# Performance work log

Measured on AMD Instinct MI355X. Metric: run time of the kernel, lower is better.

The kernel has to match this reference:

```python
import jax, jax.numpy as jnp
import numpy as np

N = 30000      # nodes
E = 480000     # edges (avg degree 16)
IN = 128       # atom in_channels
ED = 16        # edge_dim
D = 128        # hidden_channels
OUT = 64       # out_channels
L = 4          # num_layers + 1 GCNEConv layers


def setup_inputs() -> dict:
    key = jax.random.key(0)
    ks = jax.random.split(key, 8)
    w = lambda k, sh: (jax.random.normal(k, sh, dtype=jnp.float32) * 0.05)
    return {
        "x": jax.random.normal(ks[0], (N, IN), dtype=jnp.float32),
        "edge_index": jax.random.randint(ks[1], (2, E), 0, N, dtype=jnp.int64),
        "edge_attr": jax.random.normal(ks[2], (E, ED), dtype=jnp.float32),
        "W_atom": w(ks[3], (IN, D)), "b_atom": jnp.zeros((D,), jnp.float32),
        "W_bond": w(ks[4], (ED, D)), "b_bond": jnp.zeros((D,), jnp.float32),
        "W_seq": w(ks[5], (L, D, D)), "b_seq": jnp.zeros((L, D), jnp.float32),
        "W_lin": w(ks[6], (2 * D, OUT)), "b_lin": jnp.zeros((OUT,), jnp.float32),
    }


def _aggregate(h_bond, idx_i, n):
    # CMPNN 'message_booster': elementwise sum_agg * max_agg over incoming edges
    sum_agg = jax.ops.segment_sum(h_bond, idx_i, num_segments=n)
    max_agg = jax.ops.segment_max(h_bond, idx_i, num_segments=n)
    max_agg = jnp.where(jnp.isfinite(max_agg), max_agg, 0.0)  # empty segments -> 0
    return sum_agg * max_agg


def reference(x, edge_index, edge_attr, W_atom, b_atom, W_bond, b_bond,
              W_seq, b_seq, W_lin, b_lin):
    n = x.shape[0]
    idx_i = edge_index[0]  # flow='target_to_source' -> i is edge_index[0]
    idx_j = edge_index[1]

    x_proj = jax.nn.relu(x @ W_atom + b_atom)          # [N, D]
    h_atom = x_proj
    h_bond = jax.nn.relu(edge_attr @ W_bond + b_bond)  # [E, D]

    # first L-1 convs: node update + edge update
    for l in range(L - 1):
        msg = _aggregate(h_bond, idx_i, n)             # [N, D]
        h_atom = h_atom * msg                          # inner_product communicator
        # edge_update: x[edge_index_i] - edge_attr[edge_index_j] (node-index gather
        # into edge tensor, faithful to the original code; valid since E > N)
        bond = h_atom[idx_i] - h_bond[idx_j]           # [E, D]
        h_bond = jax.nn.relu(bond @ W_seq[l] + b_seq[l])

    # last conv: only the node output is used downstream
    msg = _aggregate(h_bond, idx_i, n)
    aggr_atom_message = h_atom * msg

    # top-level communicator (inner_product): hidden_state * message
    h_atom = h_atom * aggr_atom_message
    out = jnp.concatenate([h_atom, x_proj], axis=1) @ W_lin + b_lin  # [N, OUT]
    return out
```

## Files before the change

### kernel.cpp

```cpp
#include <hip/hip_runtime.h>
#include <hip/hip_bf16.h>

#define DD 128
#define SCB 256
#define CE  512
#define CB  512

typedef __attribute__((ext_vector_type(8))) short bf16x8;
typedef __attribute__((ext_vector_type(4))) float f32x4;
typedef __attribute__((ext_vector_type(2))) _Float16 f16x2;
typedef __attribute__((ext_vector_type(8))) _Float16 f16x8;

__device__ __forceinline__ unsigned bf16_rne(float f) {
    unsigned u = __float_as_uint(f);
    return (u + 0x7fffu + ((u >> 16) & 1u)) >> 16;
}

__global__ __launch_bounds__(256)
void hist_kernel(const int* __restrict__ idx_i, int* __restrict__ cnt, int E)
{
    const int e = blockIdx.x * 256 + threadIdx.x;
    if (e < E) atomicAdd(&cnt[idx_i[e]], 1);
}

__global__ __launch_bounds__(SCB)
void scan1_kernel(const int* __restrict__ cnt, int* __restrict__ exc,
                  int* __restrict__ bsum, int n)
{
    __shared__ int s[SCB];
    const int i = blockIdx.x * SCB + (int)threadIdx.x;
    const int v = (i < n) ? cnt[i] : 0;
    s[threadIdx.x] = v;
    __syncthreads();
    #pragma unroll
    for (int off = 1; off < SCB; off <<= 1) {
        int t = (threadIdx.x >= off) ? s[threadIdx.x - off] : 0;
        __syncthreads();
        s[threadIdx.x] += t;
        __syncthreads();
    }
    if (i < n) exc[i] = s[threadIdx.x] - v;
    if (threadIdx.x == SCB - 1) bsum[blockIdx.x] = s[threadIdx.x];
}

__global__ __launch_bounds__(SCB)
void scan2_kernel(int* __restrict__ bsum, int nb)
{
    __shared__ int s[SCB];
    const int v = (threadIdx.x < nb) ? bsum[threadIdx.x] : 0;
    s[threadIdx.x] = v;
    __syncthreads();
    #pragma unroll
    for (int off = 1; off < SCB; off <<= 1) {
        int t = (threadIdx.x >= off) ? s[threadIdx.x - off] : 0;
        __syncthreads();
        s[threadIdx.x] += t;
        __syncthreads();
    }
    if (threadIdx.x < nb) bsum[threadIdx.x] = s[threadIdx.x] - v;
}

__global__ __launch_bounds__(SCB)
void scan3_kernel(int* __restrict__ exc, const int* __restrict__ bsum, int n)
{
    const int i = blockIdx.x * SCB + (int)threadIdx.x;
    if (i < n) exc[i] += bsum[i >> 8];
}

__global__ __launch_bounds__(256)
void scatter_kernel(const int* __restrict__ idx_i, const int* __restrict__ idx_j,
                    int* __restrict__ cursor, int* __restrict__ perm,
                    int* __restrict__ si, int* __restrict__ sj, int E)
{
    const int e = blockIdx.x * 256 + threadIdx.x;
    if (e < E) {
        const int n = idx_i[e];
        const int p = atomicAdd(&cursor[n], 1);
        perm[p] = e;
        si[p] = n;
        sj[p] = idx_j[e];
    }
}

__global__ __launch_bounds__(512, 4)
void gemm128_mfma_kernel(float* __restrict__ A0, const float* __restrict__ A1,
                         int nA, int nTotal,
                         const float* __restrict__ W, const float* __restrict__ bias,
                         int bias_limit, int do_relu, int update,
                         float* __restrict__ sum_agg, int* __restrict__ max_agg,
                         float* __restrict__ out0, float* __restrict__ out1,
                         int ntiles)
{
    __shared__ __align__(16) unsigned char SM[65536];
    char* const Ahi = (char*)SM;
    char* const Alo = (char*)SM + 32768;

    const int t = (int)threadIdx.x;
    const int w = t >> 6;
    const int l = t & 63;
    const int g = l >> 4;
    const int q = l & 15;
    const int colv = w * 16 + q;

    bf16x8 wh[4], wl[4];
    #pragma unroll
    for (int ks = 0; ks < 4; ++ks) {
        unsigned h8[8], l8[8];
        #pragma unroll
        for (int j = 0; j < 8; ++j) {
            const float w0 = W[(size_t)(ks * 32 + g * 8 + j) * DD + colv];
            const unsigned hb = bf16_rne(w0);
            h8[j] = hb;
            l8[j] = bf16_rne(w0 - __uint_as_float(hb << 16));
        }
        uint4 ph, pl;
        ph.x = h8[0] | (h8[1] << 16); ph.y = h8[2] | (h8[3] << 16);
        ph.z = h8[4] | (h8[5] << 16); ph.w = h8[6] | (h8[7] << 16);
        pl.x = l8[0] | (l8[1] << 16); pl.y = l8[2] | (l8[3] << 16);
        pl.z = l8[4] | (l8[5] << 16); pl.w = l8[6] | (l8[7] << 16);
        wh[ks] = *(bf16x8*)&ph;
        wl[ks] = *(bf16x8*)&pl;
    }
    const float bv = bias ? bias[colv] : 0.f;

    for (int tile = blockIdx.x; tile < ntiles; tile += gridDim.x) {
        const int e0 = tile * 128;
        __syncthreads();

        #pragma unroll
        for (int i = 0; i < 4; ++i) {
            const int task = t + i * 512;
            const int row  = task >> 4;
            const int c    = task & 15;
            const int rr = min(e0 + row, nTotal - 1);
            float d[8];
            if (rr < nA) {
                float* ph0 = A0 + (size_t)rr * DD + c * 8;
                const float4 a0 = *(const float4*)ph0;
                const float4 a1 = *(const float4*)(ph0 + 4);
                if (update) {
                    float* sp = sum_agg + (size_t)rr * DD + c * 8;
                    int*   mp = max_agg + (size_t)rr * DD + c * 8;
                    const float4 s0 = *(const float4*)sp;
                    const float4 s1 = *(const float4*)(sp + 4);
                    const int4   m0 = *(const int4*)mp;
                    const int4   m1 = *(const int4*)(mp + 4);
                    d[0] = a0.x * s0.x * __int_as_float(m0.x);
                    d[1] = a0.y * s0.y * __int_as_float(m0.y);
                    d[2] = a0.z * s0.z * __int_as_float(m0.z);
                    d[3] = a0.w * s0.w * __int_as_float(m0.w);
                    d[4] = a1.x * s1.x * __int_as_float(m1.x);
                    d[5] = a1.y * s1.y * __int_as_float(m1.y);
                    d[6] = a1.z * s1.z * __int_as_float(m1.z);
                    d[7] = a1.w * s1.w * __int_as_float(m1.w);
                    *(float4*)ph0       = make_float4(d[0], d[1], d[2], d[3]);
                    *(float4*)(ph0 + 4) = make_float4(d[4], d[5], d[6], d[7]);
                    *(float4*)sp       = make_float4(0.f, 0.f, 0.f, 0.f);
                    *(float4*)(sp + 4) = make_float4(0.f, 0.f, 0.f, 0.f);
                    *(int4*)mp       = make_int4(0, 0, 0, 0);
                    *(int4*)(mp + 4) = make_int4(0, 0, 0, 0);
                } else {
                    d[0] = a0.x; d[1] = a0.y; d[2] = a0.z; d[3] = a0.w;
                    d[4] = a1.x; d[5] = a1.y; d[6] = a1.z; d[7] = a1.w;
                }
            } else {
                const float* pa = A1 + (size_t)(rr - nA) * DD + c * 8;
                const float4 a0 = *(const float4*)pa;
                const float4 a1 = *(const float4*)(pa + 4);
                d[0] = a0.x; d[1] = a0.y; d[2] = a0.z; d[3] = a0.w;
                d[4] = a1.x; d[5] = a1.y; d[6] = a1.z; d[7] = a1.w;
            }
            unsigned h8[8], l8[8];
            #pragma unroll
            for (int j = 0; j < 8; ++j) {
                const unsigned hb = bf16_rne(d[j]);
                h8[j] = hb;
                l8[j] = bf16_rne(d[j] - __uint_as_float(hb << 16));
            }
            uint4 ph, pl;
            ph.x = h8[0] | (h8[1] << 16); ph.y = h8[2] | (h8[3] << 16);
            ph.z = h8[4] | (h8[5] << 16); ph.w = h8[6] | (h8[7] << 16);
            pl.x = l8[0] | (l8[1] << 16); pl.y = l8[2] | (l8[3] << 16);
            pl.z = l8[4] | (l8[5] << 16); pl.w = l8[6] | (l8[7] << 16);
            const int off = ((row * 256 + c * 16)) ^ ((row & 7) << 4);
            *(uint4*)(Ahi + off) = ph;
            *(uint4*)(Alo + off) = pl;
        }
        __syncthreads();

        f32x4 acc[8];
        const f32x4 zero = {0.f, 0.f, 0.f, 0.f};
        #pragma unroll
        for (int m = 0; m < 8; ++m) acc[m] = zero;

        #pragma unroll
        for (int ks = 0; ks < 4; ++ks) {
            const int kbyte = ks * 64 + g * 16;
            #pragma unroll
            for (int m = 0; m < 8; ++m) {
                const int row = m * 16 + q;
                const int off = (row * 256 + kbyte) ^ ((row & 7) << 4);
                const bf16x8 ah = *(const bf16x8*)(Ahi + off);
                const bf16x8 al = *(const bf16x8*)(Alo + off);
                acc[m] = __builtin_amdgcn_mfma_f32_16x16x32_bf16(ah, wh[ks], acc[m], 0, 0, 0);
                acc[m] = __builtin_amdgcn_mfma_f32_16x16x32_bf16(ah, wl[ks], acc[m], 0, 0, 0);
                acc[m] = __builtin_amdgcn_mfma_f32_16x16x32_bf16(al, wh[ks], acc[m], 0, 0, 0);
            }
        }

        #pragma unroll
        for (int m = 0; m < 8; ++m) {
            #pragma unroll
            for (int r = 0; r < 4; ++r) {
                const int row = e0 + m * 16 + g * 4 + r;
                if (row < nTotal) {
                    float v = acc[m][r] + ((row < bias_limit) ? bv : 0.f);
                    if (do_relu) v = fmaxf(v, 0.f);
                    out0[(size_t)row * DD + colv] = v;
                    if (out1) out1[(size_t)row * DD + colv] = v;
                }
            }
        }
    }
}

__global__ __launch_bounds__(512)
void bond_pass_kernel(const float* __restrict__ edge_attr,
                      const float* __restrict__ Wb, const float* __restrict__ bb,
                      const int* __restrict__ si, const int* __restrict__ perm,
                      float* __restrict__ h_head0,
                      float* __restrict__ sum_agg, int* __restrict__ max_agg,
                      int E, int N)
{
    __shared__ __align__(16) _Float16 ea_s[CB][16];
    __shared__ int si_s[CB], pm_s[CB];

    const int p0b = blockIdx.x * CB;
    if (p0b >= E) return;
    const int t = (int)threadIdx.x;

    for (int i = t; i < CB; i += 512) {
        const int p = min(p0b + i, E - 1);
        si_s[i] = si[p];
        pm_s[i] = perm[p];
    }
    for (int task = t; task < CB * 2; task += 512) {
        const int row = task >> 1;
        const int h8i = task & 1;
        const int p = min(p0b + row, E - 1);
        const int orig = perm[p];
        const float4 a0 = *(const float4*)(edge_attr + (size_t)orig * 16 + h8i * 8);
        const float4 a1 = *(const float4*)(edge_attr + (size_t)orig * 16 + h8i * 8 + 4);
        f16x8 hv;
        hv[0] = (_Float16)a0.x; hv[1] = (_Float16)a0.y;
        hv[2] = (_Float16)a0.z; hv[3] = (_Float16)a0.w;
        hv[4] = (_Float16)a1.x; hv[5] = (_Float16)a1.y;
        hv[6] = (_Float16)a1.z; hv[7] = (_Float16)a1.w;
        *(f16x8*)(&ea_s[row][h8i * 8]) = hv;
    }
    __syncthreads();

    const int w    = t >> 6;
    const int lane = t & 63;
    const int c    = lane * 2;
    const int q0   = w * 64;
    const int pg0  = p0b + q0;
    if (pg0 >= E) return;

    f16x2 w0h[8], w1h[8];
    #pragma unroll
    for (int k = 0; k < 8; ++k) {
        const float2 wa = *(const float2*)(Wb + (2 * k)     * DD + c);
        const float2 wb2 = *(const float2*)(Wb + (2 * k + 1) * DD + c);
        w0h[k][0] = (_Float16)wa.x; w0h[k][1] = (_Float16)wb2.x;
        w1h[k][0] = (_Float16)wa.y; w1h[k][1] = (_Float16)wb2.y;
    }
    const float2 bc = *(const float2*)(bb + c);

    const int firstNode = si_s[q0];
    const int lastNode  = si_s[q0 + 63];

    int curNode = firstNode;
    float2 rs = make_float2(0.f, 0.f), rm = make_float2(0.f, 0.f);

    #define BP_FLUSH()                                                           \
    {                                                                            \
        if (curNode == firstNode || curNode == lastNode) {                       \
            atomicAdd(&sum_agg[(size_t)curNode * DD + c],     rs.x);             \
            atomicAdd(&sum_agg[(size_t)curNode * DD + c + 1], rs.y);             \
            atomicMax(&max_agg[(size_t)curNode * DD + c],     __float_as_int(rm.x)); \
            atomicMax(&max_agg[(size_t)curNode * DD + c + 1], __float_as_int(rm.y)); \
        } else {                                                                 \
            *(float2*)(sum_agg + (size_t)curNode * DD + c) = rs;                 \
            *(int2*)(max_agg + (size_t)curNode * DD + c) =                       \
                make_int2(__float_as_int(rm.x), __float_as_int(rm.y));           \
        }                                                                        \
    }

    #pragma unroll 4
    for (int kk = 0; kk < 64; ++kk) {
        const int i = si_s[q0 + kk];
        if (i != curNode) {
            BP_FLUSH();
            curNode = i;
            rs = make_float2(0.f, 0.f);
            rm = make_float2(0.f, 0.f);
        }
        const f16x8 e0 = *(const f16x8*)(&ea_s[q0 + kk][0]);
        const f16x8 e1 = *(const f16x8*)(&ea_s[q0 + kk][8]);
        float ax = bc.x, ay = bc.y;
        f16x2 p2;
        p2[0] = e0[0]; p2[1] = e0[1];
        ax = __builtin_amdgcn_fdot2(p2, w0h[0], ax, false);
        ay = __builtin_amdgcn_fdot2(p2, w1h[0], ay, false);
        p2[0] = e0[2]; p2[1] = e0[3];
        ax = __builtin_amdgcn_fdot2(p2, w0h[1], ax, false);
        ay = __builtin_amdgcn_fdot2(p2, w1h[1], ay, false);
        p2[0] = e0[4]; p2[1] = e0[5];
        ax = __builtin_amdgcn_fdot2(p2, w0h[2], ax, false);
        ay = __builtin_amdgcn_fdot2(p2, w1h[2], ay, false);
        p2[0] = e0[6]; p2[1] = e0[7];
        ax = __builtin_amdgcn_fdot2(p2, w0h[3], ax, false);
        ay = __builtin_amdgcn_fdot2(p2, w1h[3], ay, false);
        p2[0] = e1[0]; p2[1] = e1[1];
        ax = __builtin_amdgcn_fdot2(p2, w0h[4], ax, false);
        ay = __builtin_amdgcn_fdot2(p2, w1h[4], ay, false);
        p2[0] = e1[2]; p2[1] = e1[3];
        ax = __builtin_amdgcn_fdot2(p2, w0h[5], ax, false);
        ay = __builtin_amdgcn_fdot2(p2, w1h[5], ay, false);
        p2[0] = e1[4]; p2[1] = e1[5];
        ax = __builtin_amdgcn_fdot2(p2, w0h[6], ax, false);
        ay = __builtin_amdgcn_fdot2(p2, w1h[6], ay, false);
        p2[0] = e1[6]; p2[1] = e1[7];
        ax = __builtin_amdgcn_fdot2(p2, w0h[7], ax, false);
        ay = __builtin_amdgcn_fdot2(p2, w1h[7], ay, false);
        float2 v;
        v.x = fmaxf(ax, 0.f);
        v.y = fmaxf(ay, 0.f);
        if (pg0 + kk >= E) { v.x = 0.f; v.y = 0.f; }
        rs.x += v.x; rs.y += v.y;
        rm.x = fmaxf(rm.x, v.x); rm.y = fmaxf(rm.y, v.y);
        if (pg0 + kk < E) {
            const int orig = pm_s[q0 + kk];
            if (orig < N) *(float2*)(h_head0 + (size_t)orig * DD + c) = v;
        }
    }
    BP_FLUSH();
    #undef BP_FLUSH
}

__global__ __launch_bounds__(512)
void edge_pass_kernel(const float* __restrict__ PQ,
                      const int* __restrict__ si, const int* __restrict__ sj,
                      const int* __restrict__ perm,
                      float* __restrict__ head_next, int store_head,
                      float* __restrict__ sum_agg, int* __restrict__ max_agg,
                      int E, int N)
{
    __shared__ int si_s[CE], sj_s[CE], pm_s[CE];
    const int p0b = blockIdx.x * CE;
    if (p0b >= E) return;
    const int t = (int)threadIdx.x;
    for (int i = t; i < CE; i += 512) {
        const int p = min(p0b + i, E - 1);
        si_s[i] = si[p];
        sj_s[i] = sj[p];
        pm_s[i] = perm[p];
    }
    __syncthreads();

    const int w    = t >> 6;
    const int lane = t & 63;
    const int c    = lane * 2;
    const int q0   = w * 64;
    const int pg0  = p0b + q0;
    if (pg0 >= E) return;

    const int firstNode = si_s[q0];
    const int lastNode  = si_s[q0 + 63];

    const float* __restrict__ Qbase = PQ + (size_t)N * DD + c;

    float2 qa = *(const float2*)(Qbase + (size_t)sj_s[q0 + 0] * DD);
    float2 qb = *(const float2*)(Qbase + (size_t)sj_s[q0 + 1] * DD);
    float2 qc = *(const float2*)(Qbase + (size_t)sj_s[q0 + 2] * DD);
    float2 qd = *(const float2*)(Qbase + (size_t)sj_s[q0 + 3] * DD);
    float2 qe = *(const float2*)(Qbase + (size_t)sj_s[q0 + 4] * DD);
    float2 qf = *(const float2*)(Qbase + (size_t)sj_s[q0 + 5] * DD);
    float2 qg = *(const float2*)(Qbase + (size_t)sj_s[q0 + 6] * DD);
    float2 qh = *(const float2*)(Qbase + (size_t)sj_s[q0 + 7] * DD);

    int curNode = firstNode;
    float2 Pi = *(const float2*)(PQ + (size_t)curNode * DD + c);
    float2 rs = make_float2(0.f, 0.f), rm = make_float2(0.f, 0.f);

    #define EP_FLUSH()                                                           \
    {                                                                            \
        if (curNode == firstNode || curNode == lastNode) {                       \
            atomicAdd(&sum_agg[(size_t)curNode * DD + c],     rs.x);             \
            atomicAdd(&sum_agg[(size_t)curNode * DD + c + 1], rs.y);             \
            atomicMax(&max_agg[(size_t)curNode * DD + c],     __float_as_int(rm.x)); \
            atomicMax(&max_agg[(size_t)curNode * DD + c + 1], __float_as_int(rm.y)); \
        } else {                                                                 \
            *(float2*)(sum_agg + (size_t)curNode * DD + c) = rs;                 \
            *(int2*)(max_agg + (size_t)curNode * DD + c) =                       \
                make_int2(__float_as_int(rm.x), __float_as_int(rm.y));           \
        }                                                                        \
    }

    #define EP_STEP(K, QREG)                                                     \
    {                                                                            \
        const int kk = (K);                                                      \
        const int i = si_s[q0 + kk];                                             \
        if (i != curNode) {                                                      \
            EP_FLUSH();                                                          \
            curNode = i;                                                         \
            Pi = *(const float2*)(PQ + (size_t)i * DD + c);                      \
            rs = make_float2(0.f, 0.f);                                          \
            rm = make_float2(0.f, 0.f);                                          \
        }                                                                        \
        float2 v;                                                                \
        v.x = fmaxf(Pi.x - QREG.x, 0.f);                                         \
        v.y = fmaxf(Pi.y - QREG.y, 0.f);                                         \
        if (pg0 + kk >= E) { v.x = 0.f; v.y = 0.f; }                             \
        rs.x += v.x; rs.y += v.y;                                                \
        rm.x = fmaxf(rm.x, v.x); rm.y = fmaxf(rm.y, v.y);                        \
        if (store_head && (pg0 + kk) < E) {                                      \
            const int orig = pm_s[q0 + kk];                                      \
            if (orig < N) *(float2*)(head_next + (size_t)orig * DD + c) = v;     \
        }                                                                        \
        if (kk + 8 < 64)                                                         \
            QREG = *(const float2*)(Qbase + (size_t)sj_s[q0 + kk + 8] * DD);     \
    }

    #pragma unroll
    for (int k = 0; k < 64; k += 8) {
        EP_STEP(k + 0, qa);
        EP_STEP(k + 1, qb);
        EP_STEP(k + 2, qc);
        EP_STEP(k + 3, qd);
        EP_STEP(k + 4, qe);
        EP_STEP(k + 5, qf);
        EP_STEP(k + 6, qg);
        EP_STEP(k + 7, qh);
    }
    EP_FLUSH();
    #undef EP_STEP
    #undef EP_FLUSH
}

__global__ __launch_bounds__(512, 2)
void final_mfma_kernel(const float* __restrict__ h, const float* __restrict__ sum_agg,
                       const int* __restrict__ max_agg, const float* __restrict__ xp,
                       const float* __restrict__ Wl, const float* __restrict__ bl,
                       float* __restrict__ out, int N)
{
    __shared__ __align__(16) unsigned char SM[65808];
    char*  const Whi = (char*)SM;
    char*  const Wlo = (char*)SM + 32768;
    float* const Wf  = (float*)SM;
    float* const bs  = (float*)(SM + 65536);

    const int t = (int)threadIdx.x;
    {
        const float4* Wg = (const float4*)Wl;
        float4* Wd = (float4*)Wf;
        #pragma unroll
        for (int i = 0; i < 8; ++i) Wd[t + i * 512] = Wg[t + i * 512];
        if (t < 64) bs[t] = bl[t];
    }
    __syncthreads();
    {
        const int col = t & 63;
        const int kb  = (t >> 6) * 32;
        float v[32];
        #pragma unroll
        for (int j = 0; j < 32; ++j) v[j] = Wf[(size_t)(kb + j) * 64 + col];
        __syncthreads();
        #pragma unroll
        for (int c = 0; c < 4; ++c) {
            unsigned h8[8], l8[8];
            #pragma unroll
            for (int j = 0; j < 8; ++j) {
                const float w0 = v[c * 8 + j];
                const unsigned hb = bf16_rne(w0);
                h8[j] = hb;
                l8[j] = bf16_rne(w0 - __uint_as_float(hb << 16));
            }
            uint4 ph, pl;
            ph.x = h8[0] | (h8[1] << 16); ph.y = h8[2] | (h8[3] << 16);
            ph.z = h8[4] | (h8[5] << 16); ph.w = h8[6] | (h8[7] << 16);
            pl.x = l8[0] | (l8[1] << 16); pl.y = l8[2] | (l8[3] << 16);
            pl.z = l8[4] | (l8[5] << 16); pl.w = l8[6] | (l8[7] << 16);
            const int off = (col * 512 + (kb + c * 8) * 2) ^ ((col & 7) << 4);
            *(uint4*)(Whi + off) = ph;
            *(uint4*)(Wlo + off) = pl;
        }
    }
    __syncthreads();

    const int w  = t >> 6;
    const int l  = t & 63;
    const int wm = w >> 1;
    const int wn = w & 1;
    const int g  = l >> 4;
    const int q  = l & 15;
    const int r0 = (int)blockIdx.x * 128;

    f32x4 acc[2][2];
    const f32x4 zero = {0.f, 0.f, 0.f, 0.f};
    acc[0][0] = zero; acc[0][1] = zero; acc[1][0] = zero; acc[1][1] = zero;

    #pragma unroll
    for (int ks = 0; ks < 8; ++ks) {
        const int kf = (ks & 3) * 32 + g * 8;
        bf16x8 ah[2], al[2];
        #pragma unroll
        for (int m = 0; m < 2; ++m) {
            const int rr = min(r0 + wm * 32 + m * 16 + q, N - 1);
            float d[8];
            if (ks < 4) {
                const float* ph = h       + (size_t)rr * DD + kf;
                const float* ps = sum_agg + (size_t)rr * DD + kf;
                const int*   pm = max_agg + (size_t)rr * DD + kf;
                const float4 a0 = *(const float4*)ph;
                const float4 a1 = *(const float4*)(ph + 4);
                const float4 s0 = *(const float4*)ps;
                const float4 s1 = *(const float4*)(ps + 4);
                const int4   i0 = *(const int4*)pm;
                const int4   i1 = *(const int4*)(pm + 4);
                d[0] = a0.x * a0.x * s0.x * __int_as_float(i0.x);
                d[1] = a0.y * a0.y * s0.y * __int_as_float(i0.y);
                d[2] = a0.z * a0.z * s0.z * __int_as_float(i0.z);
                d[3] = a0.w * a0.w * s0.w * __int_as_float(i0.w);
                d[4] = a1.x * a1.x * s1.x * __int_as_float(i1.x);
                d[5] = a1.y * a1.y * s1.y * __int_as_float(i1.y);
                d[6] = a1.z * a1.z * s1.z * __int_as_float(i1.z);
                d[7] = a1.w * a1.w * s1.w * __int_as_float(i1.w);
            } else {
                const float* pa = xp + (size_t)rr * DD + kf;
                const float4 a0 = *(const float4*)pa;
                const float4 a1 = *(const float4*)(pa + 4);
                d[0] = a0.x; d[1] = a0.y; d[2] = a0.z; d[3] = a0.w;
                d[4] = a1.x; d[5] = a1.y; d[6] = a1.z; d[7] = a1.w;
            }
            unsigned h8[8], l8[8];
            #pragma unroll
            for (int j = 0; j < 8; ++j) {
                const unsigned hb = bf16_rne(d[j]);
                h8[j] = hb;
                l8[j] = bf16_rne(d[j] - __uint_as_float(hb << 16));
            }
            uint4 ph2, pl2;
            ph2.x = h8[0] | (h8[1] << 16); ph2.y = h8[2] | (h8[3] << 16);
            ph2.z = h8[4] | (h8[5] << 16); ph2.w = h8[6] | (h8[7] << 16);
            pl2.x = l8[0] | (l8[1] << 16); pl2.y = l8[2] | (l8[3] << 16);
            pl2.z = l8[4] | (l8[5] << 16); pl2.w = l8[6] | (l8[7] << 16);
            ah[m] = *(bf16x8*)&ph2;
            al[m] = *(bf16x8*)&pl2;
        }
        bf16x8 bh[2], blo[2];
        #pragma unroll
        for (int n = 0; n < 2; ++n) {
            const int colv = wn * 32 + n * 16 + q;
            const int off = (colv * 512 + ks * 64 + g * 16) ^ ((colv & 7) << 4);
            bh[n]  = *(const bf16x8*)(Whi + off);
            blo[n] = *(const bf16x8*)(Wlo + off);
        }
        #pragma unroll
        for (int m = 0; m < 2; ++m)
            #pragma unroll
            for (int n = 0; n < 2; ++n) {
                acc[m][n] = __builtin_amdgcn_mfma_f32_16x16x32_bf16(ah[m], bh[n],  acc[m][n], 0, 0, 0);
                acc[m][n] = __builtin_amdgcn_mfma_f32_16x16x32_bf16(ah[m], blo[n], acc[m][n], 0, 0, 0);
                acc[m][n] = __builtin_amdgcn_mfma_f32_16x16x32_bf16(al[m], bh[n],  acc[m][n], 0, 0, 0);
            }
    }

    #pragma unroll
    for (int n = 0; n < 2; ++n) {
        const int colv = wn * 32 + n * 16 + q;
        const float bv = bs[colv];
        #pragma unroll
        for (int m = 0; m < 2; ++m) {
            #pragma unroll
            for (int r = 0; r < 4; ++r) {
                const int row = r0 + wm * 32 + m * 16 + g * 4 + r;
                if (row < N) out[(size_t)row * 64 + colv] = acc[m][n][r] + bv;
            }
        }
    }
}

extern "C" void kernel_launch(void* const* d_in, const int* in_sizes, int n_in,
                              void* d_out, int out_size, void* d_ws, size_t ws_size,
                              hipStream_t stream)
{
    const float* x         = (const float*)d_in[0];
    const int*   edge_idx  = (const int*)d_in[1];
    const float* edge_attr = (const float*)d_in[2];
    const float* W_atom    = (const float*)d_in[3];
    const float* b_atom    = (const float*)d_in[4];
    const float* W_bond    = (const float*)d_in[5];
    const float* b_bond    = (const float*)d_in[6];
    const float* W_seq     = (const float*)d_in[7];
    const float* b_seq     = (const float*)d_in[8];
    const float* W_lin     = (const float*)d_in[9];
    const float* b_lin     = (const float*)d_in[10];
    float* out = (float*)d_out;

    const int N = in_sizes[0] / DD;
    const int E = in_sizes[1] / 2;
    const int* idx_i = edge_idx;
    const int* idx_j = edge_idx + E;

    const size_t nd = (size_t)N * DD;
    float* ws      = (float*)d_ws;
    float* x_proj  = ws;
    float* h_atom  = x_proj + nd;
    float* head    = h_atom + nd;
    float* sum_agg = head + nd;
    int*   max_agg = (int*)(sum_agg + nd);
    float* PQ      = (float*)(max_agg + nd);
    int*   cnt     = (int*)(PQ + 2 * nd);
    int*   cursor  = cnt + N;
    int*   bsum    = cursor + N;
    int*   perm    = bsum + 256;
    int*   si      = perm + E;
    int*   sj      = si + E;

    hipMemsetAsync(cnt, 0, (size_t)N * 4, stream);
    hist_kernel<<<(E + 255) / 256, 256, 0, stream>>>(idx_i, cnt, E);
    const int nb_scan = (N + SCB - 1) / SCB;
    scan1_kernel<<<nb_scan, SCB, 0, stream>>>(cnt, cursor, bsum, N);
    scan2_kernel<<<1, SCB, 0, stream>>>(bsum, nb_scan);
    scan3_kernel<<<nb_scan, SCB, 0, stream>>>(cursor, bsum, N);
    scatter_kernel<<<(E + 255) / 256, 256, 0, stream>>>(idx_i, idx_j, cursor, perm, si, sj, E);

    hipMemsetAsync(sum_agg, 0, nd * 4, stream);
    hipMemsetAsync(max_agg, 0, nd * 4, stream);

    const int ntiles_n = (N + 127) / 128;
    gemm128_mfma_kernel<<<ntiles_n, 512, 0, stream>>>(
        (float*)x, x, N, N, W_atom, b_atom, N, 1, 0, nullptr, nullptr,
        x_proj, h_atom, ntiles_n);

    bond_pass_kernel<<<(E + CB - 1) / CB, 512, 0, stream>>>(
        edge_attr, W_bond, b_bond, si, perm, head, sum_agg, max_agg, E, N);

    const int ntiles_pq = (2 * N + 127) / 128;
    const int ep_blocks = (E + CE - 1) / CE;
    for (int l = 0; l < 3; ++l) {
        gemm128_mfma_kernel<<<ntiles_pq, 512, 0, stream>>>(
            h_atom, head, N, 2 * N, W_seq + (size_t)l * DD * DD,
            b_seq + (size_t)l * DD, N, 0, 1, sum_agg, max_agg,
            PQ, nullptr, ntiles_pq);
        edge_pass_kernel<<<ep_blocks, 512, 0, stream>>>(
            PQ, si, sj, perm, head, (l < 2) ? 1 : 0, sum_agg, max_agg, E, N);
    }

    final_mfma_kernel<<<(N + 127) / 128, 512, 0, stream>>>(
        h_atom, sum_agg, (const int*)max_agg, x_proj, W_lin, b_lin, out, N);
}
```

Measured before the change: 387.4 us.

## Fuse atom projection GEMM and bond pass into one launch

Merges the atom-projection GEMM and the bond-pass kernel into a single launch, assigning the first block range to GEMM tiles and the remainder to bond-pass tiles. The two stages are independent, so they can now run concurrently and one kernel launch and its tail drain are removed. The cost is a shared 64KB LDS allocation for every block and a launch bound of 4 blocks per CU, which may reduce occupancy for the bond-pass blocks that need far less LDS.

New measurement: 384.3 us. Within noise of the previous version (-0.8%).

```diff
diff --git a/kernel.cpp b/kernel.cpp
--- a/kernel.cpp
+++ b/kernel.cpp
@@ -224,129 +224,231 @@
     }
 }
 
-__global__ __launch_bounds__(512)
-void bond_pass_kernel(const float* __restrict__ edge_attr,
+__global__ __launch_bounds__(512, 4)
+void proj_bond_kernel(const float* __restrict__ x,
+                      const float* __restrict__ W, const float* __restrict__ bias,
+                      float* __restrict__ x_proj, float* __restrict__ h_atom,
+                      int Nn, int nTilesProj,
+                      const float* __restrict__ edge_attr,
                       const float* __restrict__ Wb, const float* __restrict__ bb,
                       const int* __restrict__ si, const int* __restrict__ perm,
                       float* __restrict__ h_head0,
                       float* __restrict__ sum_agg, int* __restrict__ max_agg,
-                      int E, int N)
-{
-    __shared__ __align__(16) _Float16 ea_s[CB][16];
-    __shared__ int si_s[CB], pm_s[CB];
-
-    const int p0b = blockIdx.x * CB;
-    if (p0b >= E) return;
+                      int E)
+{
+    __shared__ __align__(16) unsigned char SM[65536];
     const int t = (int)threadIdx.x;
 
-    for (int i = t; i < CB; i += 512) {
-        const int p = min(p0b + i, E - 1);
-        si_s[i] = si[p];
-        pm_s[i] = perm[p];
-    }
-    for (int task = t; task < CB * 2; task += 512) {
-        const int row = task >> 1;
-        const int h8i = task & 1;
-        const int p = min(p0b + row, E - 1);
-        const int orig = perm[p];
-        const float4 a0 = *(const float4*)(edge_attr + (size_t)orig * 16 + h8i * 8);
-        const float4 a1 = *(const float4*)(edge_attr + (size_t)orig * 16 + h8i * 8 + 4);
-        f16x8 hv;
-        hv[0] = (_Float16)a0.x; hv[1] = (_Float16)a0.y;
-        hv[2] = (_Float16)a0.z; hv[3] = (_Float16)a0.w;
-        hv[4] = (_Float16)a1.x; hv[5] = (_Float16)a1.y;
-        hv[6] = (_Float16)a1.z; hv[7] = (_Float16)a1.w;
-        *(f16x8*)(&ea_s[row][h8i * 8]) = hv;
-    }
-    __syncthreads();
-
-    const int w    = t >> 6;
-    const int lane = t & 63;
-    const int c    = lane * 2;
-    const int q0   = w * 64;
-    const int pg0  = p0b + q0;
-    if (pg0 >= E) return;
-
-    f16x2 w0h[8], w1h[8];
-    #pragma unroll
-    for (int k = 0; k < 8; ++k) {
-        const float2 wa = *(const float2*)(Wb + (2 * k)     * DD + c);
-        const float2 wb2 = *(const float2*)(Wb + (2 * k + 1) * DD + c);
-        w0h[k][0] = (_Float16)wa.x; w0h[k][1] = (_Float16)wb2.x;
-        w1h[k][0] = (_Float16)wa.y; w1h[k][1] = (_Float16)wb2.y;
-    }
-    const float2 bc = *(const float2*)(bb + c);
-
-    const int firstNode = si_s[q0];
-    const int lastNode  = si_s[q0 + 63];
-
-    int curNode = firstNode;
-    float2 rs = make_float2(0.f, 0.f), rm = make_float2(0.f, 0.f);
-
-    #define BP_FLUSH()                                                           \
-    {                                                                            \
-        if (curNode == firstNode || curNode == lastNode) {                       \
-            atomicAdd(&sum_agg[(size_t)curNode * DD + c],     rs.x);             \
-            atomicAdd(&sum_agg[(size_t)curNode * DD + c + 1], rs.y);             \
-            atomicMax(&max_agg[(size_t)curNode * DD + c],     __float_as_int(rm.x)); \
-            atomicMax(&max_agg[(size_t)curNode * DD + c + 1], __float_as_int(rm.y)); \
-        } else {                                                                 \
-            *(float2*)(sum_agg + (size_t)curNode * DD + c) = rs;                 \
-            *(int2*)(max_agg + (size_t)curNode * DD + c) =                       \
-                make_int2(__float_as_int(rm.x), __float_as_int(rm.y));           \
-        }                                                                        \
-    }
-
-    #pragma unroll 4
-    for (int kk = 0; kk < 64; ++kk) {
-        const int i = si_s[q0 + kk];
-        if (i != curNode) {
-            BP_FLUSH();
-            curNode = i;
-            rs = make_float2(0.f, 0.f);
-            rm = make_float2(0.f, 0.f);
-        }
-        const f16x8 e0 = *(const f16x8*)(&ea_s[q0 + kk][0]);
-        const f16x8 e1 = *(const f16x8*)(&ea_s[q0 + kk][8]);
-        float ax = bc.x, ay = bc.y;
-        f16x2 p2;
-        p2[0] = e0[0]; p2[1] = e0[1];
-        ax = __builtin_amdgcn_fdot2(p2, w0h[0], ax, false);
-        ay = __builtin_amdgcn_fdot2(p2, w1h[0], ay, false);
-        p2[0] = e0[2]; p2[1] = e0[3];
-        ax = __builtin_amdgcn_fdot2(p2, w0h[1], ax, false);
-        ay = __builtin_amdgcn_fdot2(p2, w1h[1], ay, false);
-        p2[0] = e0[4]; p2[1] = e0[5];
-        ax = __builtin_amdgcn_fdot2(p2, w0h[2], ax, false);
-        ay = __builtin_amdgcn_fdot2(p2, w1h[2], ay, false);
-        p2[0] = e0[6]; p2[1] = e0[7];
-        ax = __builtin_amdgcn_fdot2(p2, w0h[3], ax, false);
-        ay = __builtin_amdgcn_fdot2(p2, w1h[3], ay, false);
-        p2[0] = e1[0]; p2[1] = e1[1];
-        ax = __builtin_amdgcn_fdot2(p2, w0h[4], ax, false);
-        ay = __builtin_amdgcn_fdot2(p2, w1h[4], ay, false);
-        p2[0] = e1[2]; p2[1] = e1[3];
-        ax = __builtin_amdgcn_fdot2(p2, w0h[5], ax, false);
-        ay = __builtin_amdgcn_fdot2(p2, w1h[5], ay, false);
-        p2[0] = e1[4]; p2[1] = e1[5];
-        ax = __builtin_amdgcn_fdot2(p2, w0h[6], ax, false);
-        ay = __builtin_amdgcn_fdot2(p2, w1h[6], ay, false);
-        p2[0] = e1[6]; p2[1] = e1[7];
-        ax = __builtin_amdgcn_fdot2(p2, w0h[7], ax, false);
-        ay = __builtin_amdgcn_fdot2(p2, w1h[7], ay, false);
-        float2 v;
-        v.x = fmaxf(ax, 0.f);
-        v.y = fmaxf(ay, 0.f);
-        if (pg0 + kk >= E) { v.x = 0.f; v.y = 0.f; }
-        rs.x += v.x; rs.y += v.y;
-        rm.x = fmaxf(rm.x, v.x); rm.y = fmaxf(rm.y, v.y);
-        if (pg0 + kk < E) {
-            const int orig = pm_s[q0 + kk];
-            if (orig < N) *(float2*)(h_head0 + (size_t)orig * DD + c) = v;
-        }
-    }
-    BP_FLUSH();
-    #undef BP_FLUSH
+    if ((int)blockIdx.x < nTilesProj) {
+        char* const Ahi = (char*)SM;
+        char* const Alo = (char*)SM + 32768;
+        const int w = t >> 6;
+        const int l = t & 63;
+        const int g = l >> 4;
+        const int q = l & 15;
+        const int colv = w * 16 + q;
+
+        bf16x8 wh[4], wl[4];
+        #pragma unroll
+        for (int ks = 0; ks < 4; ++ks) {
+            unsigned h8[8], l8[8];
+            #pragma unroll
+            for (int j = 0; j < 8; ++j) {
+                const float w0 = W[(size_t)(ks * 32 + g * 8 + j) * DD + colv];
+                const unsigned hb = bf16_rne(w0);
+                h8[j] = hb;
+                l8[j] = bf16_rne(w0 - __uint_as_float(hb << 16));
+            }
+            uint4 ph, pl;
+            ph.x = h8[0] | (h8[1] << 16); ph.y = h8[2] | (h8[3] << 16);
+            ph.z = h8[4] | (h8[5] << 16); ph.w = h8[6] | (h8[7] << 16);
+            pl.x = l8[0] | (l8[1] << 16); pl.y = l8[2] | (l8[3] << 16);
+            pl.z = l8[4] | (l8[5] << 16); pl.w = l8[6] | (l8[7] << 16);
+            wh[ks] = *(bf16x8*)&ph;
+            wl[ks] = *(bf16x8*)&pl;
+        }
+        const float bv = bias[colv];
+
+        const int e0 = (int)blockIdx.x * 128;
+
+        #pragma unroll
+        for (int i = 0; i < 4; ++i) {
+            const int task = t + i * 512;
+            const int row  = task >> 4;
+            const int c    = task & 15;
+            const int rr = min(e0 + row, Nn - 1);
+            const float* pa = x + (size_t)rr * DD + c * 8;
+            const float4 a0 = *(const float4*)pa;
+            const float4 a1 = *(const float4*)(pa + 4);
+            float d[8] = {a0.x, a0.y, a0.z, a0.w, a1.x, a1.y, a1.z, a1.w};
+            unsigned h8[8], l8[8];
+            #pragma unroll
+            for (int j = 0; j < 8; ++j) {
+                const unsigned hb = bf16_rne(d[j]);
+                h8[j] = hb;
+                l8[j] = bf16_rne(d[j] - __uint_as_float(hb << 16));
+            }
+            uint4 ph, pl;
+            ph.x = h8[0] | (h8[1] << 16); ph.y = h8[2] | (h8[3] << 16);
+            ph.z = h8[4] | (h8[5] << 16); ph.w = h8[6] | (h8[7] << 16);
+            pl.x = l8[0] | (l8[1] << 16); pl.y = l8[2] | (l8[3] << 16);
+            pl.z = l8[4] | (l8[5] << 16); pl.w = l8[6] | (l8[7] << 16);
+            const int off = ((row * 256 + c * 16)) ^ ((row & 7) << 4);
+            *(uint4*)(Ahi + off) = ph;
+            *(uint4*)(Alo + off) = pl;
+        }
+        __syncthreads();
+
+        f32x4 acc[8];
+        const f32x4 zero = {0.f, 0.f, 0.f, 0.f};
+        #pragma unroll
+        for (int m = 0; m < 8; ++m) acc[m] = zero;
+
+        #pragma unroll
+        for (int ks = 0; ks < 4; ++ks) {
+            const int kbyte = ks * 64 + g * 16;
+            #pragma unroll
+            for (int m = 0; m < 8; ++m) {
+                const int row = m * 16 + q;
+                const int off = (row * 256 + kbyte) ^ ((row & 7) << 4);
+                const bf16x8 ah = *(const bf16x8*)(Ahi + off);
+                const bf16x8 al = *(const bf16x8*)(Alo + off);
+                acc[m] = __builtin_amdgcn_mfma_f32_16x16x32_bf16(ah, wh[ks], acc[m], 0, 0, 0);
+                acc[m] = __builtin_amdgcn_mfma_f32_16x16x32_bf16(ah, wl[ks], acc[m], 0, 0, 0);
+                acc[m] = __builtin_amdgcn_mfma_f32_16x16x32_bf16(al, wh[ks], acc[m], 0, 0, 0);
+            }
+        }
+
+        #pragma unroll
+        for (int m = 0; m < 8; ++m) {
+            #pragma unroll
+            for (int r = 0; r < 4; ++r) {
+                const int row = e0 + m * 16 + g * 4 + r;
+                if (row < Nn) {
+                    const float v = fmaxf(acc[m][r] + bv, 0.f);
+                    x_proj[(size_t)row * DD + colv] = v;
+                    h_atom[(size_t)row * DD + colv] = v;
+                }
+            }
+        }
+    } else {
+        _Float16* const ea_s = (_Float16*)SM;
+        int* const si_s = (int*)(SM + 16384);
+        int* const pm_s = (int*)(SM + 18432);
+
+        const int bid = (int)blockIdx.x - nTilesProj;
+        const int p0b = bid * CB;
+        if (p0b >= E) return;
+
+        for (int i = t; i < CB; i += 512) {
+            const int p = min(p0b + i, E - 1);
+            si_s[i] = si[p];
+            pm_s[i] = perm[p];
+        }
+        for (int task = t; task < CB * 2; task += 512) {
+            const int row = task >> 1;
+            const int h8i = task & 1;
+            const int p = min(p0b + row, E - 1);
+            const int orig = perm[p];
+            const float4 a0 = *(const float4*)(edge_attr + (size_t)orig * 16 + h8i * 8);
+            const float4 a1 = *(const float4*)(edge_attr + (size_t)orig * 16 + h8i * 8 + 4);
+            f16x8 hv;
+            hv[0] = (_Float16)a0.x; hv[1] = (_Float16)a0.y;
+            hv[2] = (_Float16)a0.z; hv[3] = (_Float16)a0.w;
+            hv[4] = (_Float16)a1.x; hv[5] = (_Float16)a1.y;
+            hv[6] = (_Float16)a1.z; hv[7] = (_Float16)a1.w;
+            *(f16x8*)(&ea_s[row * 16 + h8i * 8]) = hv;
+        }
+        __syncthreads();
+
+        const int w    = t >> 6;
+        const int lane = t & 63;
+        const int c    = lane * 2;
+        const int q0   = w * 64;
+        const int pg0  = p0b + q0;
+        if (pg0 >= E) return;
+
+        f16x2 w0h[8], w1h[8];
+        #pragma unroll
+        for (int k = 0; k < 8; ++k) {
+            const float2 wa  = *(const float2*)(Wb + (2 * k)     * DD + c);
+            const float2 wb2 = *(const float2*)(Wb + (2 * k + 1) * DD + c);
+            w0h[k][0] = (_Float16)wa.x; w0h[k][1] = (_Float16)wb2.x;
+            w1h[k][0] = (_Float16)wa.y; w1h[k][1] = (_Float16)wb2.y;
+        }
+        const float2 bc = *(const float2*)(bb + c);
+
+        const int firstNode = si_s[q0];
+        const int lastNode  = si_s[q0 + 63];
+
+        int curNode = firstNode;
+        float2 rs = make_float2(0.f, 0.f), rm = make_float2(0.f, 0.f);
+
+        #define BP_FLUSH()                                                       \
+        {                                                                        \
+            if (curNode == firstNode || curNode == lastNode) {                   \
+                atomicAdd(&sum_agg[(size_t)curNode * DD + c],     rs.x);         \
+                atomicAdd(&sum_agg[(size_t)curNode * DD + c + 1], rs.y);         \
+                atomicMax(&max_agg[(size_t)curNode * DD + c],     __float_as_int(rm.x)); \
+                atomicMax(&max_agg[(size_t)curNode * DD + c + 1], __float_as_int(rm.y)); \
+            } else {                                                             \
+                *(float2*)(sum_agg + (size_t)curNode * DD + c) = rs;             \
+                *(int2*)(max_agg + (size_t)curNode * DD + c) =                   \
+                    make_int2(__float_as_int(rm.x), __float_as_int(rm.y));       \
+            }                                                                    \
+        }
+
+        #pragma unroll 4
+        for (int kk = 0; kk < 64; ++kk) {
+            const int i = si_s[q0 + kk];
+            if (i != curNode) {
+                BP_FLUSH();
+                curNode = i;
+                rs = make_float2(0.f, 0.f);
+                rm = make_float2(0.f, 0.f);
+            }
+            const f16x8 e0 = *(const f16x8*)(&ea_s[(q0 + kk) * 16]);
+            const f16x8 e1 = *(const f16x8*)(&ea_s[(q0 + kk) * 16 + 8]);
+            float ax = bc.x, ay = bc.y;
+            f16x2 p2;
+            p2[0] = e0[0]; p2[1] = e0[1];
+            ax = __builtin_amdgcn_fdot2(p2, w0h[0], ax, false);
+            ay = __builtin_amdgcn_fdot2(p2, w1h[0], ay, false);
+            p2[0] = e0[2]; p2[1] = e0[3];
+            ax = __builtin_amdgcn_fdot2(p2, w0h[1], ax, false);
+            ay = __builtin_amdgcn_fdot2(p2, w1h[1], ay, false);
+            p2[0] = e0[4]; p2[1] = e0[5];
+            ax = __builtin_amdgcn_fdot2(p2, w0h[2], ax, false);
+            ay = __builtin_amdgcn_fdot2(p2, w1h[2], ay, false);
+            p2[0] = e0[6]; p2[1] = e0[7];
+            ax = __builtin_amdgcn_fdot2(p2, w0h[3], ax, false);
+            ay = __builtin_amdgcn_fdot2(p2, w1h[3], ay, false);
+            p2[0] = e1[0]; p2[1] = e1[1];
+            ax = __builtin_amdgcn_fdot2(p2, w0h[4], ax, false);
+            ay = __builtin_amdgcn_fdot2(p2, w1h[4], ay, false);
+            p2[0] = e1[2]; p2[1] = e1[3];
+            ax = __builtin_amdgcn_fdot2(p2, w0h[5], ax, false);
+            ay = __builtin_amdgcn_fdot2(p2, w1h[5], ay, false);
+            p2[0] = e1[4]; p2[1] = e1[5];
+            ax = __builtin_amdgcn_fdot2(p2, w0h[6], ax, false);
+            ay = __builtin_amdgcn_fdot2(p2, w1h[6], ay, false);
+            p2[0] = e1[6]; p2[1] = e1[7];
+            ax = __builtin_amdgcn_fdot2(p2, w0h[7], ax, false);
+            ay = __builtin_amdgcn_fdot2(p2, w1h[7], ay, false);
+            float2 v;
+            v.x = fmaxf(ax, 0.f);
+            v.y = fmaxf(ay, 0.f);
+            if (pg0 + kk >= E) { v.x = 0.f; v.y = 0.f; }
+            rs.x += v.x; rs.y += v.y;
+            rm.x = fmaxf(rm.x, v.x); rm.y = fmaxf(rm.y, v.y);
+            if (pg0 + kk < E) {
+                const int orig = pm_s[q0 + kk];
+                if (orig < Nn) *(float2*)(h_head0 + (size_t)orig * DD + c) = v;
+            }
+        }
+        BP_FLUSH();
+        #undef BP_FLUSH
+    }
 }
 
 __global__ __launch_bounds__(512)
@@ -640,13 +742,11 @@
     hipMemsetAsync(sum_agg, 0, nd * 4, stream);
     hipMemsetAsync(max_agg, 0, nd * 4, stream);
 
-    const int ntiles_n = (N + 127) / 128;
-    gemm128_mfma_kernel<<<ntiles_n, 512, 0, stream>>>(
-        (float*)x, x, N, N, W_atom, b_atom, N, 1, 0, nullptr, nullptr,
-        x_proj, h_atom, ntiles_n);
-
-    bond_pass_kernel<<<(E + CB - 1) / CB, 512, 0, stream>>>(
-        edge_attr, W_bond, b_bond, si, perm, head, sum_agg, max_agg, E, N);
+    const int ntiles_n   = (N + 127) / 128;
+    const int bond_blocks = (E + CB - 1) / CB;
+    proj_bond_kernel<<<ntiles_n + bond_blocks, 512, 0, stream>>>(
+        x, W_atom, b_atom, x_proj, h_atom, N, ntiles_n,
+        edge_attr, W_bond, b_bond, si, perm, head, sum_agg, max_agg, E);
 
     const int ntiles_pq = (2 * N + 127) / 128;
     const int ep_blocks = (E + CE - 1) / CE;
```
